# Optimization experiments

Hardware: AMD Instinct MI355X
Metric: run time of the kernel (lower is better)

## Reference

```python
import jax, jax.numpy as jnp
import numpy as np

T, H, I = 32768, 2048, 768  # tokens, hidden_size, moe_intermediate_size


def setup_inputs() -> dict:
    key = jax.random.key(0)
    k1, k2, k3 = jax.random.split(key, 3)
    hidden_states = jax.random.normal(k1, (T, H), dtype=jnp.float32)
    # merged gate_up weight: columns [0:I] = gate, [I:2I] = up
    w_gate_up = jax.random.normal(k2, (H, 2 * I), dtype=jnp.float32) * 0.02
    w_down = jax.random.normal(k3, (I, H), dtype=jnp.float32) * 0.02
    return {"hidden_states": hidden_states, "w_gate_up": w_gate_up, "w_down": w_down}


def reference(hidden_states, w_gate_up, w_down):
    # gate_up projection: [T, H] @ [H, 2I] -> [T, 2I]
    gate_up = jnp.einsum('th,hf->tf', hidden_states, w_gate_up)
    gate, up = jnp.split(gate_up, 2, axis=-1)
    # SiluAndMul: silu(gate) * up -> [T, I]
    x = jax.nn.silu(gate) * up
    # down projection: [T, I] @ [I, H] -> [T, H]
    return jnp.einsum('ti,ih->th', x, w_down)
```

## Files before the change

kernel.cpp:

```cpp
#include <hip/hip_runtime.h>

#define T_TOK 32768
#define H_DIM 2048
#define I_DIM 768
#define N1_DIM 1536

typedef unsigned short ushort_t;
typedef __attribute__((ext_vector_type(8))) short  short8;
typedef __attribute__((ext_vector_type(4))) float  floatx4;

__device__ __forceinline__ ushort_t f2bf(float f) {
    union { float f; unsigned u; } v; v.f = f;
    unsigned u = v.u;
    unsigned r = (u + 0x7fffu + ((u >> 16) & 1u)) >> 16;
    return (ushort_t)r;
}

typedef __attribute__((address_space(1))) const void gq_t;
typedef __attribute__((address_space(3))) void lq_t;
__device__ __forceinline__ void gld_lds16(const void* g, void* l) {
    __builtin_amdgcn_global_load_lds((gq_t*)g, (lq_t*)l, 16, 0, 0);
}

__global__ __launch_bounds__(256) void cast_f32_bf16_k(
    const float* __restrict__ in, ushort_t* __restrict__ out)
{
    size_t i = ((size_t)blockIdx.x * 256 + threadIdx.x) * 8;
    const float4 a = *(const float4*)(in + i);
    const float4 b = *(const float4*)(in + i + 4);
    short8 o;
    o[0] = (short)f2bf(a.x); o[1] = (short)f2bf(a.y);
    o[2] = (short)f2bf(a.z); o[3] = (short)f2bf(a.w);
    o[4] = (short)f2bf(b.x); o[5] = (short)f2bf(b.y);
    o[6] = (short)f2bf(b.z); o[7] = (short)f2bf(b.w);
    *(short8*)(out + i) = o;
}

__device__ __forceinline__ int gu_perm(int c) {
    const int t  = (c >= I_DIM) ? 1 : 0;
    const int cc = c - t * I_DIM;
    return ((cc >> 4) << 5) + (t << 4) + (cc & 15);
}

template <bool PERM>
__global__ __launch_bounds__(256) void transpose_cast_k(
    const float* __restrict__ in, ushort_t* __restrict__ out, int R, int C)
{
    __shared__ float tile[32][33];
    const int c0 = blockIdx.x * 32;
    const int r0 = blockIdx.y * 32;
    const int tx = threadIdx.x;
    const int ty = threadIdx.y;
#pragma unroll
    for (int dy = 0; dy < 32; dy += 8)
        tile[ty + dy][tx] = in[(size_t)(r0 + ty + dy) * C + (c0 + tx)];
    __syncthreads();
#pragma unroll
    for (int dy = 0; dy < 32; dy += 8) {
        const int c = c0 + ty + dy;
        const int orow = PERM ? gu_perm(c) : c;
        out[(size_t)orow * R + (r0 + tx)] = f2bf(tile[tx][ty + dy]);
    }
}

#define GB    __builtin_amdgcn_s_barrier()
#define SB0   __builtin_amdgcn_sched_barrier(0)
#define LGKM0 asm volatile("s_waitcnt lgkmcnt(0)" ::: "memory")
#define VMW(N) asm volatile("s_waitcnt vmcnt(" #N ")" ::: "memory")

template <int EPI>
__global__ __launch_bounds__(512, 2) void gemm_bt8(
    const ushort_t* __restrict__ A,
    const ushort_t* __restrict__ Bt,
    void* __restrict__ Cv,
    int lda, int ldb, int ldc, int K)
{
    __shared__ __align__(16) ushort_t lds[65536];

    const int tid  = threadIdx.x;
    const int lane = tid & 63;
    const int wave = tid >> 6;
    const int wm   = (wave >> 2) * 128;
    const int wn   = (wave & 3) * 64;
    const int s    = lane & 15;
    const int q    = lane >> 4;

    const int nwg = gridDim.x;
    const int cpx = nwg >> 3;
    const int wg  = blockIdx.x;
    const int swz = (wg & 7) * cpx + (wg >> 3);
    const int m0  = (swz & 127) * 256;
    const int n0  = (swz >> 7) * 256;

    const int srow = wave * 16 + (lane >> 2);
    const int scol = (lane & 3) * 8;
    const ushort_t* Ab = A  + (size_t)(m0 + srow) * lda + scol;
    const ushort_t* Bb = Bt + (size_t)(n0 + srow) * ldb + scol;
    ushort_t* ldsA = &lds[wave * 512];
    ushort_t* ldsB = &lds[32768 + wave * 512];

#define STAGE_A(kt, h, c, b) gld_lds16(Ab + (size_t)((c)*128) * lda + (kt) + (h)*32, \
                                       ldsA + ((b)*2 + (h)) * 8192 + (c)*4096)
#define STAGE_B(kt, h, c, b) gld_lds16(Bb + (size_t)((c)*128) * ldb + (kt) + (h)*32, \
                                       ldsB + ((b)*2 + (h)) * 8192 + (c)*4096)

    const int arow = wm + s;
    const int brow = wn + s;
#define LDA4(b, ks, mh, av) { _Pragma("unroll") for (int ii = 0; ii < 4; ++ii) \
    av[ii] = *(const short8*)&lds[((b)*2 + (ks)) * 8192 + (arow + (mh)*64 + ii*16) * 32 + q*8]; }
#define LDB4(b, ks, bv) { _Pragma("unroll") for (int jj = 0; jj < 4; ++jj) \
    bv[jj] = *(const short8*)&lds[32768 + ((b)*2 + (ks)) * 8192 + (brow + jj*16) * 32 + q*8]; }
#define MFMA16(mh, av, bv) { _Pragma("unroll") for (int ii = 0; ii < 4; ++ii) \
    _Pragma("unroll") for (int jj = 0; jj < 4; ++jj) \
        acc[(mh)*4 + ii][jj] = __builtin_amdgcn_mfma_f32_16x16x32_bf16( \
            av[ii], bv[jj], acc[(mh)*4 + ii][jj], 0, 0, 0); }

    floatx4 acc[8][4];
#pragma unroll
    for (int i = 0; i < 8; ++i)
#pragma unroll
        for (int j = 0; j < 4; ++j)
            acc[i][j] = floatx4{0.f, 0.f, 0.f, 0.f};

    const int NT = K >> 6;

    STAGE_A(0, 0, 0, 0); STAGE_A(0, 0, 1, 0);
    STAGE_B(0, 0, 0, 0); STAGE_B(0, 0, 1, 0);
    STAGE_A(0, 1, 0, 0); STAGE_A(0, 1, 1, 0);
    STAGE_B(0, 1, 0, 0); STAGE_B(0, 1, 1, 0);
    VMW(4);
    GB; SB0;

    for (int t = 0; t < NT - 1; ++t) {
        const int b   = t & 1;
        const int nb  = b ^ 1;
        const int kt1 = (t + 1) << 6;
        short8 av[4], bv[4];
        LDA4(b, 0, 0, av); LDB4(b, 0, bv);
        STAGE_A(kt1, 0, 0, nb); STAGE_A(kt1, 0, 1, nb);
        GB; LGKM0; SB0;
        __builtin_amdgcn_s_setprio(1); MFMA16(0, av, bv); __builtin_amdgcn_s_setprio(0);
        GB;
        LDA4(b, 0, 1, av);
        STAGE_B(kt1, 0, 0, nb); STAGE_B(kt1, 0, 1, nb);
        GB; LGKM0; SB0;
        __builtin_amdgcn_s_setprio(1); MFMA16(1, av, bv); __builtin_amdgcn_s_setprio(0);
        VMW(4);
        GB;
        LDA4(b, 1, 0, av); LDB4(b, 1, bv);
        STAGE_A(kt1, 1, 0, nb); STAGE_A(kt1, 1, 1, nb);
        GB; LGKM0; SB0;
        __builtin_amdgcn_s_setprio(1); MFMA16(0, av, bv); __builtin_amdgcn_s_setprio(0);
        GB;
        LDA4(b, 1, 1, av);
        STAGE_B(kt1, 1, 0, nb); STAGE_B(kt1, 1, 1, nb);
        GB; LGKM0; SB0;
        __builtin_amdgcn_s_setprio(1); MFMA16(1, av, bv); __builtin_amdgcn_s_setprio(0);
        VMW(4);
        GB;
    }
    {
        const int b = (NT - 1) & 1;
        short8 av[4], bv[4];
        LDA4(b, 0, 0, av); LDB4(b, 0, bv);
        GB; LGKM0; SB0;
        __builtin_amdgcn_s_setprio(1); MFMA16(0, av, bv); __builtin_amdgcn_s_setprio(0);
        GB;
        LDA4(b, 0, 1, av);
        GB; LGKM0; SB0;
        __builtin_amdgcn_s_setprio(1); MFMA16(1, av, bv); __builtin_amdgcn_s_setprio(0);
        VMW(0);
        GB;
        LDA4(b, 1, 0, av); LDB4(b, 1, bv);
        GB; LGKM0; SB0;
        __builtin_amdgcn_s_setprio(1); MFMA16(0, av, bv); __builtin_amdgcn_s_setprio(0);
        GB;
        LDA4(b, 1, 1, av);
        LGKM0; SB0;
        __builtin_amdgcn_s_setprio(1); MFMA16(1, av, bv); __builtin_amdgcn_s_setprio(0);
    }

    if (EPI == 0) {
        float* C = (float*)Cv;
#pragma unroll
        for (int i = 0; i < 8; ++i) {
            const int r = m0 + wm + i * 16 + q * 4;
#pragma unroll
            for (int j = 0; j < 4; ++j) {
                const int cn = n0 + wn + j * 16 + s;
#pragma unroll
                for (int tt = 0; tt < 4; ++tt)
                    C[(size_t)(r + tt) * ldc + cn] = acc[i][j][tt];
            }
        }
    } else {
        ushort_t* X = (ushort_t*)Cv;
        const int cb2 = (n0 + wn) >> 1;
#pragma unroll
        for (int i = 0; i < 8; ++i) {
            const int r = m0 + wm + i * 16 + q * 4;
#pragma unroll
            for (int jp = 0; jp < 2; ++jp) {
                const int cn = cb2 + jp * 16 + s;
#pragma unroll
                for (int tt = 0; tt < 4; ++tt) {
                    const float g  = acc[i][2 * jp][tt];
                    const float u  = acc[i][2 * jp + 1][tt];
                    const float sv = g / (1.0f + __expf(-g));
                    X[(size_t)(r + tt) * ldc + cn] = f2bf(sv * u);
                }
            }
        }
    }
#undef STAGE_A
#undef STAGE_B
#undef LDA4
#undef LDB4
#undef MFMA16
}

extern "C" void kernel_launch(void* const* d_in, const int* in_sizes, int n_in,
                              void* d_out, int out_size, void* d_ws, size_t ws_size,
                              hipStream_t stream)
{
    const float* hs  = (const float*)d_in[0];
    const float* wgu = (const float*)d_in[1];
    const float* wd  = (const float*)d_in[2];
    float*       out = (float*)d_out;

    char* ws = (char*)d_ws;
    ushort_t* wgu_t = (ushort_t*)ws;
    ushort_t* wd_t  = (ushort_t*)(ws + 6291456);
    ushort_t* xb    = (ushort_t*)(ws + 9437184);

    ushort_t* hs_b = (ushort_t*)d_out;

    cast_f32_bf16_k<<<32768, 256, 0, stream>>>(hs, hs_b);
    transpose_cast_k<true><<<dim3(N1_DIM / 32, H_DIM / 32), dim3(32, 8), 0, stream>>>(
        wgu, wgu_t, H_DIM, N1_DIM);
    transpose_cast_k<false><<<dim3(H_DIM / 32, I_DIM / 32), dim3(32, 8), 0, stream>>>(
        wd, wd_t, I_DIM, H_DIM);
    gemm_bt8<1><<<(T_TOK / 256) * (N1_DIM / 256), 512, 0, stream>>>(
        hs_b, wgu_t, (void*)xb, H_DIM, H_DIM, I_DIM, H_DIM);
    gemm_bt8<0><<<(T_TOK / 256) * (H_DIM / 256), 512, 0, stream>>>(
        xb, wd_t, (void*)out, I_DIM, I_DIM, H_DIM, I_DIM);
}
```

Before: 748.3 us.

## Use XOR-swizzled 64-wide LDS tiles and N-major block mapping in GEMM

Changes the LDS staging layout from two 32-column half-tiles to one 64-column row per K-step, with XOR swizzling of 16-byte chunks to avoid bank conflicts on MFMA operand reads. The staging order and vmcnt waits are reshuffled so A and B loads interleave across the four sub-phases. Block-to-tile mapping now puts N tiles of the same M row on consecutive blocks, which improves A-tile L2 reuse. This risks a different global access pattern per wave (8 rows × 128B) and a correctness hazard if the wait counts do not cover the reordered loads.

After: 716.3 us. 4.3% less time.

```diff
diff --git a/kernel.cpp b/kernel.cpp
--- a/kernel.cpp
+++ b/kernel.cpp
@@ -68,7 +68,7 @@
 #define LGKM0 asm volatile("s_waitcnt lgkmcnt(0)" ::: "memory")
 #define VMW(N) asm volatile("s_waitcnt vmcnt(" #N ")" ::: "memory")
 
-template <int EPI>
+template <int EPI, int NBN>
 __global__ __launch_bounds__(512, 2) void gemm_bt8(
     const ushort_t* __restrict__ A,
     const ushort_t* __restrict__ Bt,
@@ -84,36 +84,38 @@
     const int wn   = (wave & 3) * 64;
     const int s    = lane & 15;
     const int q    = lane >> 4;
+    const int s7   = s & 7;
 
     const int nwg = gridDim.x;
     const int cpx = nwg >> 3;
     const int wg  = blockIdx.x;
     const int swz = (wg & 7) * cpx + (wg >> 3);
-    const int m0  = (swz & 127) * 256;
-    const int n0  = (swz >> 7) * 256;
-
-    const int srow = wave * 16 + (lane >> 2);
-    const int scol = (lane & 3) * 8;
-    const ushort_t* Ab = A  + (size_t)(m0 + srow) * lda + scol;
-    const ushort_t* Bb = Bt + (size_t)(n0 + srow) * ldb + scol;
-    ushort_t* ldsA = &lds[wave * 512];
-    ushort_t* ldsB = &lds[32768 + wave * 512];
-
-#define STAGE_A(kt, h, c, b) gld_lds16(Ab + (size_t)((c)*128) * lda + (kt) + (h)*32, \
-                                       ldsA + ((b)*2 + (h)) * 8192 + (c)*4096)
-#define STAGE_B(kt, h, c, b) gld_lds16(Bb + (size_t)((c)*128) * ldb + (kt) + (h)*32, \
-                                       ldsB + ((b)*2 + (h)) * 8192 + (c)*4096)
+    const int mb  = swz / NBN;
+    const int m0  = mb * 256;
+    const int n0  = (swz - mb * NBN) * 256;
+
+    const int r3 = lane >> 3;
+    const int sk = ((lane & 7) ^ r3) * 8;
+    const ushort_t* Ab = A  + (size_t)(m0 + wave * 8 + r3) * lda + sk;
+    const ushort_t* Bb = Bt + (size_t)(n0 + wave * 8 + r3) * ldb + sk;
+
+#define STAGE_A(kt, ofs, b) gld_lds16(Ab + (size_t)((ofs) * 8) * lda + (kt), \
+                                      &lds[(b) * 16384 + (wave + (ofs)) * 512])
+#define STAGE_B(kt, ofs, b) gld_lds16(Bb + (size_t)((ofs) * 8) * ldb + (kt), \
+                                      &lds[32768 + (b) * 16384 + (wave + (ofs)) * 512])
 
     const int arow = wm + s;
     const int brow = wn + s;
 #define LDA4(b, ks, mh, av) { _Pragma("unroll") for (int ii = 0; ii < 4; ++ii) \
-    av[ii] = *(const short8*)&lds[((b)*2 + (ks)) * 8192 + (arow + (mh)*64 + ii*16) * 32 + q*8]; }
+    av[ii] = *(const short8*)&lds[(b) * 16384 + (arow + (mh) * 64 + ii * 16) * 64 \
+                                  + (((ks) * 4 + q) ^ s7) * 8]; }
 #define LDB4(b, ks, bv) { _Pragma("unroll") for (int jj = 0; jj < 4; ++jj) \
-    bv[jj] = *(const short8*)&lds[32768 + ((b)*2 + (ks)) * 8192 + (brow + jj*16) * 32 + q*8]; }
+    bv[jj] = *(const short8*)&lds[32768 + (b) * 16384 + (brow + jj * 16) * 64 \
+                                  + (((ks) * 4 + q) ^ s7) * 8]; }
 #define MFMA16(mh, av, bv) { _Pragma("unroll") for (int ii = 0; ii < 4; ++ii) \
     _Pragma("unroll") for (int jj = 0; jj < 4; ++jj) \
-        acc[(mh)*4 + ii][jj] = __builtin_amdgcn_mfma_f32_16x16x32_bf16( \
-            av[ii], bv[jj], acc[(mh)*4 + ii][jj], 0, 0, 0); }
+        acc[(mh) * 4 + ii][jj] = __builtin_amdgcn_mfma_f32_16x16x32_bf16( \
+            av[ii], bv[jj], acc[(mh) * 4 + ii][jj], 0, 0, 0); }
 
     floatx4 acc[8][4];
 #pragma unroll
@@ -124,11 +126,11 @@
 
     const int NT = K >> 6;
 
-    STAGE_A(0, 0, 0, 0); STAGE_A(0, 0, 1, 0);
-    STAGE_B(0, 0, 0, 0); STAGE_B(0, 0, 1, 0);
-    STAGE_A(0, 1, 0, 0); STAGE_A(0, 1, 1, 0);
-    STAGE_B(0, 1, 0, 0); STAGE_B(0, 1, 1, 0);
-    VMW(4);
+    STAGE_A(0, 0, 0);  STAGE_A(0, 16, 0);
+    STAGE_B(0, 0, 0);  STAGE_B(0, 8, 0);
+    STAGE_B(0, 16, 0); STAGE_B(0, 24, 0);
+    STAGE_A(0, 8, 0);  STAGE_A(0, 24, 0);
+    VMW(2);
     GB; SB0;
 
     for (int t = 0; t < NT - 1; ++t) {
@@ -137,26 +139,26 @@
         const int kt1 = (t + 1) << 6;
         short8 av[4], bv[4];
         LDA4(b, 0, 0, av); LDB4(b, 0, bv);
-        STAGE_A(kt1, 0, 0, nb); STAGE_A(kt1, 0, 1, nb);
-        GB; LGKM0; SB0;
-        __builtin_amdgcn_s_setprio(1); MFMA16(0, av, bv); __builtin_amdgcn_s_setprio(0);
+        STAGE_A(kt1, 0, nb); STAGE_A(kt1, 16, nb);
+        GB; LGKM0; SB0;
+        __builtin_amdgcn_s_setprio(1); MFMA16(0, av, bv); __builtin_amdgcn_s_setprio(0);
+        VMW(2);
         GB;
         LDA4(b, 0, 1, av);
-        STAGE_B(kt1, 0, 0, nb); STAGE_B(kt1, 0, 1, nb);
-        GB; LGKM0; SB0;
-        __builtin_amdgcn_s_setprio(1); MFMA16(1, av, bv); __builtin_amdgcn_s_setprio(0);
-        VMW(4);
+        STAGE_B(kt1, 0, nb); STAGE_B(kt1, 8, nb);
+        GB; LGKM0; SB0;
+        __builtin_amdgcn_s_setprio(1); MFMA16(1, av, bv); __builtin_amdgcn_s_setprio(0);
         GB;
         LDA4(b, 1, 0, av); LDB4(b, 1, bv);
-        STAGE_A(kt1, 1, 0, nb); STAGE_A(kt1, 1, 1, nb);
+        STAGE_B(kt1, 16, nb); STAGE_B(kt1, 24, nb);
         GB; LGKM0; SB0;
         __builtin_amdgcn_s_setprio(1); MFMA16(0, av, bv); __builtin_amdgcn_s_setprio(0);
         GB;
         LDA4(b, 1, 1, av);
-        STAGE_B(kt1, 1, 0, nb); STAGE_B(kt1, 1, 1, nb);
-        GB; LGKM0; SB0;
-        __builtin_amdgcn_s_setprio(1); MFMA16(1, av, bv); __builtin_amdgcn_s_setprio(0);
-        VMW(4);
+        STAGE_A(kt1, 8, nb); STAGE_A(kt1, 24, nb);
+        GB; LGKM0; SB0;
+        __builtin_amdgcn_s_setprio(1); MFMA16(1, av, bv); __builtin_amdgcn_s_setprio(0);
+        VMW(2);
         GB;
     }
     {
@@ -165,11 +167,11 @@
         LDA4(b, 0, 0, av); LDB4(b, 0, bv);
         GB; LGKM0; SB0;
         __builtin_amdgcn_s_setprio(1); MFMA16(0, av, bv); __builtin_amdgcn_s_setprio(0);
+        VMW(0);
         GB;
         LDA4(b, 0, 1, av);
         GB; LGKM0; SB0;
         __builtin_amdgcn_s_setprio(1); MFMA16(1, av, bv); __builtin_amdgcn_s_setprio(0);
-        VMW(0);
         GB;
         LDA4(b, 1, 0, av); LDB4(b, 1, bv);
         GB; LGKM0; SB0;
@@ -240,8 +242,8 @@
         wgu, wgu_t, H_DIM, N1_DIM);
     transpose_cast_k<false><<<dim3(H_DIM / 32, I_DIM / 32), dim3(32, 8), 0, stream>>>(
         wd, wd_t, I_DIM, H_DIM);
-    gemm_bt8<1><<<(T_TOK / 256) * (N1_DIM / 256), 512, 0, stream>>>(
+    gemm_bt8<1, 6><<<(T_TOK / 256) * (N1_DIM / 256), 512, 0, stream>>>(
         hs_b, wgu_t, (void*)xb, H_DIM, H_DIM, I_DIM, H_DIM);
-    gemm_bt8<0><<<(T_TOK / 256) * (H_DIM / 256), 512, 0, stream>>>(
+    gemm_bt8<0, 8><<<(T_TOK / 256) * (H_DIM / 256), 512, 0, stream>>>(
         xb, wd_t, (void*)out, I_DIM, I_DIM, H_DIM, I_DIM);
 }
```
